# Kernel optimization log

Hardware: AMD Instinct MI355X
Metric: run time of the kernel (lower is better)

Reference implementation:

```python
import jax, jax.numpy as jnp
import numpy as np

C = 512
B, W, H = 16, 64, 64
K = 128


def setup_inputs() -> dict:
    key = jax.random.key(0)
    ks = jax.random.split(key, 17)
    s = 0.02
    inp = {
        "x1": jax.random.normal(ks[0], (B, C, W, H), jnp.float32),
        "y1": jax.random.normal(ks[1], (B, K, C), jnp.float32),
        "x2": jax.random.normal(ks[2], (B, C, W, H), jnp.float32),
        "y2": jax.random.normal(ks[3], (B, K, C), jnp.float32),
        # 1x1 conv weights stored as [out, in]
        "wq1": jax.random.normal(ks[4], (C // 4, C), jnp.float32) * s,
        "bq1": jnp.zeros((C // 4,), jnp.float32),
        "wq2": jax.random.normal(ks[5], (C // 4, C), jnp.float32) * s,
        "bq2": jnp.zeros((C // 4,), jnp.float32),
        "wk1": jax.random.normal(ks[6], (C // 2, C), jnp.float32) * s,
        "bk1": jnp.zeros((C // 2,), jnp.float32),
        "wk2": jax.random.normal(ks[7], (C // 2, C), jnp.float32) * s,
        "bk2": jnp.zeros((C // 2,), jnp.float32),
        "wv1": jax.random.normal(ks[8], (C, C), jnp.float32) * s,
        "bv1": jnp.zeros((C,), jnp.float32),
        "wv2": jax.random.normal(ks[9], (C, C), jnp.float32) * s,
        "bv2": jnp.zeros((C,), jnp.float32),
        "scale": jnp.ones((1,), jnp.float32) * 0.5,  # nn.Parameter(zeros) would kill grads; nonzero for testing
    }
    return inp


def reference(x1, y1, x2, y2, wq1, bq1, wq2, bq2, wk1, bk1, wk2, bk2,
              wv1, bv1, wv2, bv2, scale):
    b, c, w, h = x1.shape
    n = w * h
    # 1x1 convs == channel-wise linear maps
    q1 = jnp.einsum('bcwh,dc->bdwh', x1, wq1) + bq1[None, :, None, None]
    q2 = jnp.einsum('bcwh,dc->bdwh', x2, wq2) + bq2[None, :, None, None]
    # concat along channels -> [B, C/2, N] -> [B, N, C/2]
    q = jnp.concatenate([q1, q2], axis=1).reshape(b, c // 2, n).transpose(0, 2, 1)
    k1 = y1 @ wk1.T + bk1  # [B, K, C/2]
    k2 = y2 @ wk2.T + bk2
    v1 = y1 @ wv1.T + bv1  # [B, K, C]
    v2 = y2 @ wv2.T + bv2
    e1 = jnp.einsum('bnd,bkd->bnk', q, k1)  # [B, N, K]
    e2 = jnp.einsum('bnd,bkd->bnk', q, k2)
    attn = jax.nn.softmax(jnp.abs(e1 - e2), axis=-1)
    # out = value^T @ attn^T : [B, C, N]
    o1 = jnp.einsum('bkc,bnk->bcn', v1, attn).reshape(b, c, w, h)
    o2 = jnp.einsum('bkc,bnk->bcn', v2, attn).reshape(b, c, w, h)
    out1 = scale[0] * o1 + x1
    out2 = scale[0] * o2 + x2
    return out1, out2
```

## Files before the change

kernel.cpp:

```cpp
#include <hip/hip_runtime.h>

typedef unsigned short u16;
typedef __attribute__((ext_vector_type(8))) short short8v;
typedef __attribute__((ext_vector_type(4))) float floatx4;

#define B_ 16
#define C_ 512
#define N_ 4096
#define K_ 128
#define NT 64

__device__ __forceinline__ float bf2f(u16 u) {
    unsigned int x = ((unsigned int)u) << 16;
    return __builtin_bit_cast(float, x);
}
__device__ __forceinline__ u16 f2bf(float f) {
    unsigned int u = __builtin_bit_cast(unsigned int, f);
    u = u + 0x7FFFu + ((u >> 16) & 1u);
    return (u16)(u >> 16);
}

__global__ void conv_all(const float* __restrict__ y1, const float* __restrict__ y2,
                         const float* __restrict__ wk1, const float* __restrict__ wk2,
                         const float* __restrict__ wv1, const float* __restrict__ wv2,
                         const float* __restrict__ wq1, const float* __restrict__ wq2,
                         u16* y1b, u16* y2b, u16* wk1b, u16* wk2b, u16* wv1b, u16* wv2b,
                         u16* wq1t, u16* wq2t) {
    int tid = blockIdx.x * 256 + threadIdx.x;
    const int SY = B_ * K_ * C_;
    const int SWK = 256 * 512;
    const int SWV = 512 * 512;
    const int SQ = 128 * 512;
    int base = 2*SY + 2*SWK + 2*SWV;
    if (tid < base) {
        const float* src; u16* dst; int off;
        if (tid < SY)                 { src = y1;  dst = y1b;  off = tid; }
        else if (tid < 2*SY)          { src = y2;  dst = y2b;  off = tid - SY; }
        else if (tid < 2*SY+SWK)      { src = wk1; dst = wk1b; off = tid - 2*SY; }
        else if (tid < 2*SY+2*SWK)    { src = wk2; dst = wk2b; off = tid - 2*SY - SWK; }
        else if (tid < 2*SY+2*SWK+SWV){ src = wv1; dst = wv1b; off = tid - 2*SY - 2*SWK; }
        else                          { src = wv2; dst = wv2b; off = tid - 2*SY - 2*SWK - SWV; }
        dst[off] = f2bf(src[off]);
    } else {
        int e = tid - base;
        const float* s = (e >= SQ) ? wq2 : wq1;
        u16* d = (e >= SQ) ? wq2t : wq1t;
        e &= (SQ - 1);
        int dd = e >> 9;
        int c = e & 511;
        d[c * 128 + dd] = f2bf(s[dd * 512 + c]);
    }
}

__global__ void gemm_gkgv(const u16* __restrict__ y1b, const u16* __restrict__ y2b,
                          const u16* __restrict__ wk1b, const u16* __restrict__ wk2b,
                          const u16* __restrict__ wv1b, const u16* __restrict__ wv2b,
                          const float* __restrict__ bk1, const float* __restrict__ bk2,
                          const float* __restrict__ bv1, const float* __restrict__ bv2,
                          u16* k1b, u16* k2b, u16* vt1, u16* vt2) {
    int l = threadIdx.x;
    int id = blockIdx.x;
    const u16 *A, *Bt; const float* bias; u16* outp;
    int m0, n0, po; bool bias_m;
    if (id < 256) {
        int bx = id & 1, by = (id >> 1) & 3, z = id >> 3;
        int b = z >> 1, which = z & 1;
        A = (which ? y2b : y1b) + (size_t)b * K_ * C_;
        Bt = which ? wk2b : wk1b;
        bias = which ? bk2 : bk1;
        outp = (which ? k2b : k1b) + (size_t)b * K_ * 256;
        m0 = bx * 64; n0 = by * 64; po = 256; bias_m = false;
    } else {
        int id2 = id - 256;
        int bx = id2 & 7, by = (id2 >> 3) & 1, z = id2 >> 4;
        int b = z >> 1, which = z & 1;
        A = which ? wv2b : wv1b;
        Bt = (which ? y2b : y1b) + (size_t)b * K_ * C_;
        bias = which ? bv2 : bv1;
        outp = (which ? vt2 : vt1) + (size_t)b * C_ * K_;
        m0 = bx * 64; n0 = by * 64; po = 128; bias_m = true;
    }
    floatx4 acc[4][4] = {};
    for (int ch = 0; ch < 16; ++ch) {
        int koff = ch * 32 + (l >> 4) * 8;
        short8v a[4], wv[4];
#pragma unroll
        for (int mf = 0; mf < 4; ++mf) a[mf] = *(const short8v*)(A + (size_t)(m0 + mf*16 + (l & 15)) * 512 + koff);
#pragma unroll
        for (int nf = 0; nf < 4; ++nf) wv[nf] = *(const short8v*)(Bt + (size_t)(n0 + nf*16 + (l & 15)) * 512 + koff);
#pragma unroll
        for (int mf = 0; mf < 4; ++mf)
#pragma unroll
            for (int nf = 0; nf < 4; ++nf)
                acc[mf][nf] = __builtin_amdgcn_mfma_f32_16x16x32_bf16(a[mf], wv[nf], acc[mf][nf], 0, 0, 0);
    }
#pragma unroll
    for (int mf = 0; mf < 4; ++mf)
#pragma unroll
        for (int nf = 0; nf < 4; ++nf)
#pragma unroll
            for (int rg = 0; rg < 4; ++rg) {
                int m = m0 + mf*16 + (l >> 4)*4 + rg;
                int n = n0 + nf*16 + (l & 15);
                outp[(size_t)m * po + n] = f2bf(acc[mf][nf][rg] + (bias_m ? bias[m] : bias[n]));
            }
}

__global__ void kd_sub(const u16* __restrict__ k1b, const u16* __restrict__ k2b,
                       u16* kd) {
    int tid = blockIdx.x * 256 + threadIdx.x;
    kd[tid] = f2bf(bf2f(k1b[tid]) - bf2f(k2b[tid]));
}

__global__ void ebd_k(const u16* __restrict__ kd,
                      const float* __restrict__ bq1, const float* __restrict__ bq2,
                      float* ebd) {
    int tid = blockIdx.x * 256 + threadIdx.x;
    const u16* kb = kd + (size_t)tid * 256;
    float s = 0.f;
    for (int d = 0; d < 128; ++d) s += bq1[d] * bf2f(kb[d]);
    for (int d = 0; d < 128; ++d) s += bq2[d] * bf2f(kb[128 + d]);
    ebd[tid] = s;
}

__global__ void gemm_gkk(const u16* __restrict__ kd,
                         const u16* __restrict__ wq1t, const u16* __restrict__ wq2t,
                         u16* kkd1, u16* kkd2) {
    int l = threadIdx.x;
    int z = blockIdx.z; int b = z >> 1; int which = z & 1;
    const u16* A = kd + (size_t)b * K_ * 256 + which * 128;
    const u16* Wt = which ? wq2t : wq1t;
    u16* outp = (which ? kkd2 : kkd1) + (size_t)b * K_ * C_;
    int m0 = blockIdx.x * 64, n0 = blockIdx.y * 64;
    floatx4 acc[4][4] = {};
    for (int ch = 0; ch < 4; ++ch) {
        int koff = ch * 32 + (l >> 4) * 8;
        short8v a[4], wv[4];
#pragma unroll
        for (int mf = 0; mf < 4; ++mf) a[mf] = *(const short8v*)(A + (size_t)(m0 + mf*16 + (l & 15)) * 256 + koff);
#pragma unroll
        for (int nf = 0; nf < 4; ++nf) wv[nf] = *(const short8v*)(Wt + (size_t)(n0 + nf*16 + (l & 15)) * 128 + koff);
#pragma unroll
        for (int mf = 0; mf < 4; ++mf)
#pragma unroll
            for (int nf = 0; nf < 4; ++nf)
                acc[mf][nf] = __builtin_amdgcn_mfma_f32_16x16x32_bf16(a[mf], wv[nf], acc[mf][nf], 0, 0, 0);
    }
#pragma unroll
    for (int mf = 0; mf < 4; ++mf)
#pragma unroll
        for (int nf = 0; nf < 4; ++nf)
#pragma unroll
            for (int rg = 0; rg < 4; ++rg) {
                int m = m0 + mf*16 + (l >> 4)*4 + rg;
                int n = n0 + nf*16 + (l & 15);
                outp[(size_t)m * C_ + n] = f2bf(acc[mf][nf][rg]);
            }
}

__global__ __launch_bounds__(256, 3)
void main_attn(const float* __restrict__ x1, const float* __restrict__ x2,
               const u16* __restrict__ kkd1, const u16* __restrict__ kkd2,
               const u16* __restrict__ vt1, const u16* __restrict__ vt2,
               const float* __restrict__ ebd,
               const float* __restrict__ scale_p,
               float* __restrict__ out1, float* __restrict__ out2) {
    __shared__ u16 xTb[2][4096];
    __shared__ u16 attn_s[8192];
    __shared__ float redA[256];
    __shared__ float redM[64];

    int bid0 = blockIdx.x;
    int bid = ((bid0 & 7) << 7) | (bid0 >> 3);
    int b = bid >> 6;
    int n0 = (bid & 63) * NT;
    int t = threadIdx.x;
    int w = t >> 6;
    int l = t & 63;

    const float sc = scale_p[0];
    const float* xs0 = x1 + (size_t)b * C_ * N_;
    const float* xs1 = x2 + (size_t)b * C_ * N_;
    const u16* kkp[2] = { kkd1 + (size_t)b * K_ * C_, kkd2 + (size_t)b * K_ * C_ };

    floatx4 ed[4][2] = {};

    float pvA0[8], pvA1[8], pvB0[8], pvB1[8];
    short8v kkA[2][2], kkB[2][2];

    auto LOADX = [&](int r, float (&v0)[8], float (&v1)[8]) {
        const float* xp = (r >= 8 ? xs1 : xs0) + (size_t)((r & 7) * 64 + w * 16 + (l >> 5) * 8) * N_ + n0 + 2 * (l & 31);
#pragma unroll
        for (int j = 0; j < 8; ++j) { float2 f = *(const float2*)(xp + (size_t)j * N_); v0[j] = f.x; v1[j] = f.y; }
    };
    auto LOADK = [&](int r, short8v (&kkf)[2][2]) {
        const u16* base = kkp[r >> 3] + (size_t)(w * 32 + (l & 15)) * 512 + (r & 7) * 64 + (l >> 4) * 8;
#pragma unroll
        for (int kf = 0; kf < 2; ++kf)
#pragma unroll
            for (int ch = 0; ch < 2; ++ch)
                kkf[kf][ch] = *(const short8v*)(base + kf * 16 * 512 + ch * 32);
    };
    auto WRITEXT = [&](u16* xbuf, float (&v0)[8], float (&v1)[8]) {
        short8v p0, p1;
#pragma unroll
        for (int j = 0; j < 8; ++j) { p0[j] = (short)f2bf(v0[j]); p1[j] = (short)f2bf(v1[j]); }
        int row0 = 2 * (l & 31);
        int sw = 8 * ((w * 2 + (l >> 5)) ^ ((l & 31) & 7));
        *(short8v*)&xbuf[row0 * 64 + sw] = p0;
        *(short8v*)&xbuf[(row0 + 1) * 64 + sw] = p1;
    };
    auto EMM = [&](const u16* xbuf, short8v (&kkf)[2][2]) {
#pragma unroll
        for (int ch = 0; ch < 2; ++ch) {
            short8v a[4];
#pragma unroll
            for (int mf = 0; mf < 4; ++mf) {
                int row = mf * 16 + (l & 15);
                int g = ch * 4 + (l >> 4);
                a[mf] = *(const short8v*)&xbuf[row * 64 + 8 * (g ^ ((row >> 1) & 7))];
            }
#pragma unroll
            for (int kf = 0; kf < 2; ++kf)
#pragma unroll
                for (int mf = 0; mf < 4; ++mf)
                    ed[mf][kf] = __builtin_amdgcn_mfma_f32_16x16x32_bf16(a[mf], kkf[kf][ch], ed[mf][kf], 0, 0, 0);
        }
    };

    LOADX(0, pvA0, pvA1); LOADK(0, kkA);
    WRITEXT(xTb[0], pvA0, pvA1);
    LOADX(1, pvB0, pvB1); LOADK(1, kkB);
#pragma unroll
    for (int rr = 0; rr < 8; ++rr) {
        int rA = 2 * rr, rB = 2 * rr + 1;
        __syncthreads();
        EMM(xTb[0], kkA);
        WRITEXT(xTb[1], pvB0, pvB1);
        if (rA + 2 <= 15) { LOADX(rA + 2, pvA0, pvA1); LOADK(rA + 2, kkA); }
        __syncthreads();
        EMM(xTb[1], kkB);
        if (rB + 1 <= 15) WRITEXT(xTb[0], pvA0, pvA1);
        if (rB + 2 <= 15) { LOADX(rB + 2, pvB0, pvB1); LOADK(rB + 2, kkB); }
    }

    float ebdv[2];
#pragma unroll
    for (int kf = 0; kf < 2; ++kf) ebdv[kf] = ebd[b * 128 + w * 32 + kf * 16 + (l & 15)];
#pragma unroll
    for (int mf = 0; mf < 4; ++mf)
#pragma unroll
        for (int kf = 0; kf < 2; ++kf)
#pragma unroll
            for (int rg = 0; rg < 4; ++rg)
                ed[mf][kf][rg] = fabsf(ed[mf][kf][rg] + ebdv[kf]);

    float m16[16];
#pragma unroll
    for (int mf = 0; mf < 4; ++mf)
#pragma unroll
        for (int rg = 0; rg < 4; ++rg)
            m16[mf * 4 + rg] = fmaxf(ed[mf][0][rg], ed[mf][1][rg]);
#pragma unroll
    for (int st = 1; st < 16; st <<= 1)
#pragma unroll
        for (int i = 0; i < 16; ++i)
            m16[i] = fmaxf(m16[i], __shfl_xor(m16[i], st));
    if ((l & 15) == 0) {
#pragma unroll
        for (int mf = 0; mf < 4; ++mf)
#pragma unroll
            for (int rg = 0; rg < 4; ++rg)
                redA[w * 64 + mf * 16 + (l >> 4) * 4 + rg] = m16[mf * 4 + rg];
    }
    __syncthreads();
    if (t < 64) redM[t] = fmaxf(fmaxf(redA[t], redA[64 + t]), fmaxf(redA[128 + t], redA[192 + t]));
    __syncthreads();

    float s16[16];
#pragma unroll
    for (int mf = 0; mf < 4; ++mf)
#pragma unroll
        for (int rg = 0; rg < 4; ++rg) {
            float mr = redM[mf * 16 + (l >> 4) * 4 + rg];
            float e0 = __expf(ed[mf][0][rg] - mr);
            float e1 = __expf(ed[mf][1][rg] - mr);
            ed[mf][0][rg] = e0; ed[mf][1][rg] = e1;
            s16[mf * 4 + rg] = e0 + e1;
        }
#pragma unroll
    for (int st = 1; st < 16; st <<= 1)
#pragma unroll
        for (int i = 0; i < 16; ++i)
            s16[i] += __shfl_xor(s16[i], st);
    if ((l & 15) == 0) {
#pragma unroll
        for (int mf = 0; mf < 4; ++mf)
#pragma unroll
            for (int rg = 0; rg < 4; ++rg)
                redA[w * 64 + mf * 16 + (l >> 4) * 4 + rg] = s16[mf * 4 + rg];
    }
    __syncthreads();
    if (t < 64) redM[t] = redA[t] + redA[64 + t] + redA[128 + t] + redA[192 + t];
    __syncthreads();

#pragma unroll
    for (int mf = 0; mf < 4; ++mf)
#pragma unroll
        for (int rg = 0; rg < 4; ++rg) {
            int row = mf * 16 + (l >> 4) * 4 + rg;
            float inv = 1.0f / redM[row];
#pragma unroll
            for (int kf = 0; kf < 2; ++kf) {
                int col = w * 32 + kf * 16 + (l & 15);
                attn_s[row * 128 + 8 * ((col >> 3) ^ (row & 7)) + (col & 7)] = f2bf(ed[mf][kf][rg] * inv);
            }
        }
    __syncthreads();

    const u16* vt1p = vt1 + (size_t)b * C_ * K_;
    const u16* vt2p = vt2 + (size_t)b * C_ * K_;
    float* out1p = out1 + (size_t)b * C_ * N_;
    float* out2p = out2 + (size_t)b * C_ * N_;
    for (int q = 0; q < 8; ++q) {
        int oi = q >> 2, cc = q & 3;
        const u16* vt = oi ? vt2p : vt1p;
        const float* xr = oi ? xs1 : xs0;
        float* op = oi ? out2p : out1p;
        short8v vf[2][4];
#pragma unroll
        for (int mf = 0; mf < 2; ++mf)
#pragma unroll
            for (int kc = 0; kc < 4; ++kc)
                vf[mf][kc] = *(const short8v*)(vt + (size_t)(cc * 128 + w * 32 + mf * 16 + (l & 15)) * K_ + kc * 32 + (l >> 4) * 8);
        float resv[2][4][4];
#pragma unroll
        for (int mf = 0; mf < 2; ++mf)
#pragma unroll
            for (int rg = 0; rg < 4; ++rg)
#pragma unroll
                for (int nf = 0; nf < 4; ++nf)
                    resv[mf][rg][nf] = xr[(size_t)(cc * 128 + w * 32 + mf * 16 + (l >> 4) * 4 + rg) * N_ + n0 + nf * 16 + (l & 15)];
        floatx4 o[2][4] = {};
#pragma unroll
        for (int kc = 0; kc < 4; ++kc) {
            short8v bb[4];
#pragma unroll
            for (int nf = 0; nf < 4; ++nf) {
                int nrow = nf * 16 + (l & 15);
                int g = kc * 4 + (l >> 4);
                bb[nf] = *(const short8v*)&attn_s[nrow * 128 + 8 * (g ^ (nrow & 7))];
            }
#pragma unroll
            for (int nf = 0; nf < 4; ++nf)
#pragma unroll
                for (int mf = 0; mf < 2; ++mf)
                    o[mf][nf] = __builtin_amdgcn_mfma_f32_16x16x32_bf16(vf[mf][kc], bb[nf], o[mf][nf], 0, 0, 0);
        }
#pragma unroll
        for (int mf = 0; mf < 2; ++mf)
#pragma unroll
            for (int rg = 0; rg < 4; ++rg)
#pragma unroll
                for (int nf = 0; nf < 4; ++nf) {
                    size_t idx = (size_t)(cc * 128 + w * 32 + mf * 16 + (l >> 4) * 4 + rg) * N_ + n0 + nf * 16 + (l & 15);
                    op[idx] = sc * o[mf][nf][rg] + resv[mf][rg][nf];
                }
    }
}

extern "C" void kernel_launch(void* const* d_in, const int* in_sizes, int n_in,
                              void* d_out, int out_size, void* d_ws, size_t ws_size,
                              hipStream_t stream) {
    const float* x1 = (const float*)d_in[0];
    const float* y1 = (const float*)d_in[1];
    const float* x2 = (const float*)d_in[2];
    const float* y2 = (const float*)d_in[3];
    const float* wq1 = (const float*)d_in[4];
    const float* bq1 = (const float*)d_in[5];
    const float* wq2 = (const float*)d_in[6];
    const float* bq2 = (const float*)d_in[7];
    const float* wk1 = (const float*)d_in[8];
    const float* bk1 = (const float*)d_in[9];
    const float* wk2 = (const float*)d_in[10];
    const float* bk2 = (const float*)d_in[11];
    const float* wv1 = (const float*)d_in[12];
    const float* bv1 = (const float*)d_in[13];
    const float* wv2 = (const float*)d_in[14];
    const float* bv2 = (const float*)d_in[15];
    const float* scale = (const float*)d_in[16];

    char* ws = (char*)d_ws;
    u16* y1b  = (u16*)(ws + 0);
    u16* y2b  = (u16*)(ws + 2097152);
    u16* wk1b = (u16*)(ws + 4194304);
    u16* wk2b = (u16*)(ws + 4456448);
    u16* wv1b = (u16*)(ws + 4718592);
    u16* wv2b = (u16*)(ws + 5242880);
    u16* wq1t = (u16*)(ws + 5767168);
    u16* wq2t = (u16*)(ws + 5898240);
    u16* k1b  = (u16*)(ws + 6029312);
    u16* k2b  = (u16*)(ws + 7077888);
    u16* kd   = (u16*)(ws + 8126464);
    u16* kkd1 = (u16*)(ws + 9175040);
    u16* kkd2 = (u16*)(ws + 11272192);
    u16* vt1  = (u16*)(ws + 13369344);
    u16* vt2  = (u16*)(ws + 15466496);
    float* ebd = (float*)(ws + 17563648);

    float* out1 = (float*)d_out;
    float* out2 = out1 + (size_t)B_ * C_ * N_;

    hipLaunchKernelGGL(conv_all, dim3(11776), dim3(256), 0, stream,
                       y1, y2, wk1, wk2, wv1, wv2, wq1, wq2,
                       y1b, y2b, wk1b, wk2b, wv1b, wv2b, wq1t, wq2t);
    hipLaunchKernelGGL(gemm_gkgv, dim3(768), dim3(64), 0, stream,
                       y1b, y2b, wk1b, wk2b, wv1b, wv2b, bk1, bk2, bv1, bv2,
                       k1b, k2b, vt1, vt2);
    hipLaunchKernelGGL(kd_sub, dim3(2048), dim3(256), 0, stream, k1b, k2b, kd);
    hipLaunchKernelGGL(ebd_k, dim3(8), dim3(256), 0, stream, kd, bq1, bq2, ebd);
    hipLaunchKernelGGL(gemm_gkk, dim3(2, 8, 32), dim3(64), 0, stream,
                       kd, wq1t, wq2t, kkd1, kkd2);
    hipLaunchKernelGGL(main_attn, dim3(1024), dim3(256), 0, stream,
                       x1, x2, kkd1, kkd2, vt1, vt2, ebd, scale,
                       out1, out2);
}
```

Before: 240.5 us.

## Double main_attn block to 512 threads and software-pipeline the PV stage

Raises main_attn from 4 to 8 waves per block. Each wave now takes half the rows in the energy GEMM (split by nh/kg), and the PV output stage gives each wave one output tensor and channel group. The PV stage double-buffers V fragments and residual loads across 16-row steps so loads overlap MFMAs. The aim is more latency hiding and lower per-thread register pressure. The cost is more block-wide barriers among 8 waves and a different LDS swizzle and x-load pattern with per-lane scalar loads.

```diff
diff --git a/kernel.cpp b/kernel.cpp
--- a/kernel.cpp
+++ b/kernel.cpp
@@ -158,7 +158,7 @@
             }
 }
 
-__global__ __launch_bounds__(256, 3)
+__global__ __launch_bounds__(512, 4)
 void main_attn(const float* __restrict__ x1, const float* __restrict__ x2,
                const u16* __restrict__ kkd1, const u16* __restrict__ kkd2,
                const u16* __restrict__ vt1, const u16* __restrict__ vt2,
@@ -177,195 +177,200 @@
     int t = threadIdx.x;
     int w = t >> 6;
     int l = t & 63;
+    int nh = w >> 2;
+    int kg = w & 3;
 
     const float sc = scale_p[0];
     const float* xs0 = x1 + (size_t)b * C_ * N_;
     const float* xs1 = x2 + (size_t)b * C_ * N_;
     const u16* kkp[2] = { kkd1 + (size_t)b * K_ * C_, kkd2 + (size_t)b * K_ * C_ };
 
-    floatx4 ed[4][2] = {};
-
-    float pvA0[8], pvA1[8], pvB0[8], pvB1[8];
+    floatx4 ed[2][2] = {};
+
+    float xA[8], xB[8];
     short8v kkA[2][2], kkB[2][2];
 
-    auto LOADX = [&](int r, float (&v0)[8], float (&v1)[8]) {
-        const float* xp = (r >= 8 ? xs1 : xs0) + (size_t)((r & 7) * 64 + w * 16 + (l >> 5) * 8) * N_ + n0 + 2 * (l & 31);
-#pragma unroll
-        for (int j = 0; j < 8; ++j) { float2 f = *(const float2*)(xp + (size_t)j * N_); v0[j] = f.x; v1[j] = f.y; }
+    auto LOADX = [&](int r, float (&v)[8]) {
+        const float* xp = (r >= 8 ? xs1 : xs0) + (size_t)((r & 7) * 64 + w * 8) * N_ + n0 + l;
+#pragma unroll
+        for (int j = 0; j < 8; ++j) v[j] = xp[(size_t)j * N_];
+    };
+    auto WRITEXT = [&](u16* xbuf, float (&v)[8]) {
+        short8v p;
+#pragma unroll
+        for (int j = 0; j < 8; ++j) p[j] = (short)f2bf(v[j]);
+        *(short8v*)&xbuf[l * 64 + 8 * (w ^ (l & 7))] = p;
     };
     auto LOADK = [&](int r, short8v (&kkf)[2][2]) {
-        const u16* base = kkp[r >> 3] + (size_t)(w * 32 + (l & 15)) * 512 + (r & 7) * 64 + (l >> 4) * 8;
+        const u16* base = kkp[r >> 3] + (size_t)(kg * 32 + (l & 15)) * 512 + (r & 7) * 64 + (l >> 4) * 8;
 #pragma unroll
         for (int kf = 0; kf < 2; ++kf)
 #pragma unroll
             for (int ch = 0; ch < 2; ++ch)
                 kkf[kf][ch] = *(const short8v*)(base + kf * 16 * 512 + ch * 32);
     };
-    auto WRITEXT = [&](u16* xbuf, float (&v0)[8], float (&v1)[8]) {
-        short8v p0, p1;
-#pragma unroll
-        for (int j = 0; j < 8; ++j) { p0[j] = (short)f2bf(v0[j]); p1[j] = (short)f2bf(v1[j]); }
-        int row0 = 2 * (l & 31);
-        int sw = 8 * ((w * 2 + (l >> 5)) ^ ((l & 31) & 7));
-        *(short8v*)&xbuf[row0 * 64 + sw] = p0;
-        *(short8v*)&xbuf[(row0 + 1) * 64 + sw] = p1;
-    };
     auto EMM = [&](const u16* xbuf, short8v (&kkf)[2][2]) {
 #pragma unroll
         for (int ch = 0; ch < 2; ++ch) {
-            short8v a[4];
-#pragma unroll
-            for (int mf = 0; mf < 4; ++mf) {
-                int row = mf * 16 + (l & 15);
+            short8v a[2];
+#pragma unroll
+            for (int mf = 0; mf < 2; ++mf) {
+                int row = nh * 32 + mf * 16 + (l & 15);
                 int g = ch * 4 + (l >> 4);
-                a[mf] = *(const short8v*)&xbuf[row * 64 + 8 * (g ^ ((row >> 1) & 7))];
+                a[mf] = *(const short8v*)&xbuf[row * 64 + 8 * (g ^ (row & 7))];
             }
 #pragma unroll
             for (int kf = 0; kf < 2; ++kf)
 #pragma unroll
-                for (int mf = 0; mf < 4; ++mf)
+                for (int mf = 0; mf < 2; ++mf)
                     ed[mf][kf] = __builtin_amdgcn_mfma_f32_16x16x32_bf16(a[mf], kkf[kf][ch], ed[mf][kf], 0, 0, 0);
         }
     };
 
-    LOADX(0, pvA0, pvA1); LOADK(0, kkA);
-    WRITEXT(xTb[0], pvA0, pvA1);
-    LOADX(1, pvB0, pvB1); LOADK(1, kkB);
+    LOADX(0, xA); LOADK(0, kkA);
+    WRITEXT(xTb[0], xA);
+    LOADX(1, xB); LOADK(1, kkB);
 #pragma unroll
     for (int rr = 0; rr < 8; ++rr) {
         int rA = 2 * rr, rB = 2 * rr + 1;
         __syncthreads();
         EMM(xTb[0], kkA);
-        WRITEXT(xTb[1], pvB0, pvB1);
-        if (rA + 2 <= 15) { LOADX(rA + 2, pvA0, pvA1); LOADK(rA + 2, kkA); }
+        WRITEXT(xTb[1], xB);
+        if (rA + 2 <= 15) { LOADX(rA + 2, xA); LOADK(rA + 2, kkA); }
         __syncthreads();
         EMM(xTb[1], kkB);
-        if (rB + 1 <= 15) WRITEXT(xTb[0], pvA0, pvA1);
-        if (rB + 2 <= 15) { LOADX(rB + 2, pvB0, pvB1); LOADK(rB + 2, kkB); }
+        if (rB + 1 <= 15) WRITEXT(xTb[0], xA);
+        if (rB + 2 <= 15) { LOADX(rB + 2, xB); LOADK(rB + 2, kkB); }
     }
 
     float ebdv[2];
 #pragma unroll
-    for (int kf = 0; kf < 2; ++kf) ebdv[kf] = ebd[b * 128 + w * 32 + kf * 16 + (l & 15)];
-#pragma unroll
-    for (int mf = 0; mf < 4; ++mf)
+    for (int kf = 0; kf < 2; ++kf) ebdv[kf] = ebd[b * 128 + kg * 32 + kf * 16 + (l & 15)];
+#pragma unroll
+    for (int mf = 0; mf < 2; ++mf)
 #pragma unroll
         for (int kf = 0; kf < 2; ++kf)
 #pragma unroll
             for (int rg = 0; rg < 4; ++rg)
                 ed[mf][kf][rg] = fabsf(ed[mf][kf][rg] + ebdv[kf]);
 
-    float m16[16];
-#pragma unroll
-    for (int mf = 0; mf < 4; ++mf)
+    float m8[8];
+#pragma unroll
+    for (int mf = 0; mf < 2; ++mf)
 #pragma unroll
         for (int rg = 0; rg < 4; ++rg)
-            m16[mf * 4 + rg] = fmaxf(ed[mf][0][rg], ed[mf][1][rg]);
+            m8[mf * 4 + rg] = fmaxf(ed[mf][0][rg], ed[mf][1][rg]);
 #pragma unroll
     for (int st = 1; st < 16; st <<= 1)
 #pragma unroll
-        for (int i = 0; i < 16; ++i)
-            m16[i] = fmaxf(m16[i], __shfl_xor(m16[i], st));
+        for (int i = 0; i < 8; ++i)
+            m8[i] = fmaxf(m8[i], __shfl_xor(m8[i], st));
     if ((l & 15) == 0) {
 #pragma unroll
-        for (int mf = 0; mf < 4; ++mf)
+        for (int mf = 0; mf < 2; ++mf)
 #pragma unroll
             for (int rg = 0; rg < 4; ++rg)
-                redA[w * 64 + mf * 16 + (l >> 4) * 4 + rg] = m16[mf * 4 + rg];
+                redA[kg * 64 + nh * 32 + mf * 16 + (l >> 4) * 4 + rg] = m8[mf * 4 + rg];
     }
     __syncthreads();
     if (t < 64) redM[t] = fmaxf(fmaxf(redA[t], redA[64 + t]), fmaxf(redA[128 + t], redA[192 + t]));
     __syncthreads();
 
-    float s16[16];
-#pragma unroll
-    for (int mf = 0; mf < 4; ++mf)
+    float s8[8];
+#pragma unroll
+    for (int mf = 0; mf < 2; ++mf)
 #pragma unroll
         for (int rg = 0; rg < 4; ++rg) {
-            float mr = redM[mf * 16 + (l >> 4) * 4 + rg];
+            float mr = redM[nh * 32 + mf * 16 + (l >> 4) * 4 + rg];
             float e0 = __expf(ed[mf][0][rg] - mr);
             float e1 = __expf(ed[mf][1][rg] - mr);
             ed[mf][0][rg] = e0; ed[mf][1][rg] = e1;
-            s16[mf * 4 + rg] = e0 + e1;
+            s8[mf * 4 + rg] = e0 + e1;
         }
 #pragma unroll
     for (int st = 1; st < 16; st <<= 1)
 #pragma unroll
-        for (int i = 0; i < 16; ++i)
-            s16[i] += __shfl_xor(s16[i], st);
+        for (int i = 0; i < 8; ++i)
+            s8[i] += __shfl_xor(s8[i], st);
     if ((l & 15) == 0) {
 #pragma unroll
-        for (int mf = 0; mf < 4; ++mf)
+        for (int mf = 0; mf < 2; ++mf)
 #pragma unroll
             for (int rg = 0; rg < 4; ++rg)
-                redA[w * 64 + mf * 16 + (l >> 4) * 4 + rg] = s16[mf * 4 + rg];
+                redA[kg * 64 + nh * 32 + mf * 16 + (l >> 4) * 4 + rg] = s8[mf * 4 + rg];
     }
     __syncthreads();
     if (t < 64) redM[t] = redA[t] + redA[64 + t] + redA[128 + t] + redA[192 + t];
     __syncthreads();
 
 #pragma unroll
-    for (int mf = 0; mf < 4; ++mf)
+    for (int mf = 0; mf < 2; ++mf)
 #pragma unroll
         for (int rg = 0; rg < 4; ++rg) {
-            int row = mf * 16 + (l >> 4) * 4 + rg;
+            int row = nh * 32 + mf * 16 + (l >> 4) * 4 + rg;
             float inv = 1.0f / redM[row];
 #pragma unroll
             for (int kf = 0; kf < 2; ++kf) {
-                int col = w * 32 + kf * 16 + (l & 15);
+                int col = kg * 32 + kf * 16 + (l & 15);
                 attn_s[row * 128 + 8 * ((col >> 3) ^ (row & 7)) + (col & 7)] = f2bf(ed[mf][kf][rg] * inv);
             }
         }
     __syncthreads();
 
-    const u16* vt1p = vt1 + (size_t)b * C_ * K_;
-    const u16* vt2p = vt2 + (size_t)b * C_ * K_;
-    float* out1p = out1 + (size_t)b * C_ * N_;
-    float* out2p = out2 + (size_t)b * C_ * N_;
-    for (int q = 0; q < 8; ++q) {
-        int oi = q >> 2, cc = q & 3;
-        const u16* vt = oi ? vt2p : vt1p;
+    {
+        int oi = w >> 2, cg = w & 3;
+        const u16* vt = (oi ? vt2 : vt1) + (size_t)b * C_ * K_;
         const float* xr = oi ? xs1 : xs0;
-        float* op = oi ? out2p : out1p;
-        short8v vf[2][4];
-#pragma unroll
-        for (int mf = 0; mf < 2; ++mf)
-#pragma unroll
-            for (int kc = 0; kc < 4; ++kc)
-                vf[mf][kc] = *(const short8v*)(vt + (size_t)(cc * 128 + w * 32 + mf * 16 + (l & 15)) * K_ + kc * 32 + (l >> 4) * 8);
-        float resv[2][4][4];
-#pragma unroll
-        for (int mf = 0; mf < 2; ++mf)
+        float* op = (oi ? out2 : out1) + (size_t)b * C_ * N_;
+
+        short8v vfA[4], vfB[4];
+        float rsA[4][4], rsB[4][4];
+        auto LOADPV = [&](int step, short8v (&vf)[4], float (&rs)[4][4]) {
+            int cr = cg * 128 + step * 16;
+            const u16* vp = vt + (size_t)(cr + (l & 15)) * K_ + (l >> 4) * 8;
+#pragma unroll
+            for (int kc = 0; kc < 4; ++kc) vf[kc] = *(const short8v*)(vp + kc * 32);
+            const float* rp = xr + (size_t)(cr + (l >> 4) * 4) * N_ + n0 + (l & 15);
 #pragma unroll
             for (int rg = 0; rg < 4; ++rg)
 #pragma unroll
                 for (int nf = 0; nf < 4; ++nf)
-                    resv[mf][rg][nf] = xr[(size_t)(cc * 128 + w * 32 + mf * 16 + (l >> 4) * 4 + rg) * N_ + n0 + nf * 16 + (l & 15)];
-        floatx4 o[2][4] = {};
-#pragma unroll
-        for (int kc = 0; kc < 4; ++kc) {
-            short8v bb[4];
-#pragma unroll
-            for (int nf = 0; nf < 4; ++nf) {
-                int nrow = nf * 16 + (l & 15);
-                int g = kc * 4 + (l >> 4);
-                bb[nf] = *(const short8v*)&attn_s[nrow * 128 + 8 * (g ^ (nrow & 7))];
+                    rs[rg][nf] = rp[(size_t)rg * N_ + nf * 16];
+        };
+        auto COMPPV = [&](int step, short8v (&vf)[4], float (&rs)[4][4]) {
+            floatx4 o[4] = {};
+#pragma unroll
+            for (int kc = 0; kc < 4; ++kc) {
+                short8v bb[4];
+#pragma unroll
+                for (int nf = 0; nf < 4; ++nf) {
+                    int nrow = nf * 16 + (l & 15);
+                    int g = kc * 4 + (l >> 4);
+                    bb[nf] = *(const short8v*)&attn_s[nrow * 128 + 8 * (g ^ (nrow & 7))];
+                }
+#pragma unroll
+                for (int nf = 0; nf < 4; ++nf)
+                    o[nf] = __builtin_amdgcn_mfma_f32_16x16x32_bf16(vf[kc], bb[nf], o[nf], 0, 0, 0);
             }
-#pragma unroll
-            for (int nf = 0; nf < 4; ++nf)
-#pragma unroll
-                for (int mf = 0; mf < 2; ++mf)
-                    o[mf][nf] = __builtin_amdgcn_mfma_f32_16x16x32_bf16(vf[mf][kc], bb[nf], o[mf][nf], 0, 0, 0);
+            int cr = cg * 128 + step * 16 + (l >> 4) * 4;
+#pragma unroll
+            for (int rg = 0; rg < 4; ++rg)
+#pragma unroll
+                for (int nf = 0; nf < 4; ++nf) {
+                    size_t idx = (size_t)(cr + rg) * N_ + n0 + nf * 16 + (l & 15);
+                    op[idx] = sc * o[nf][rg] + rs[rg][nf];
+                }
+        };
+
+        LOADPV(0, vfA, rsA);
+        LOADPV(1, vfB, rsB);
+#pragma unroll
+        for (int ss = 0; ss < 4; ++ss) {
+            COMPPV(2 * ss, vfA, rsA);
+            if (2 * ss + 2 < 8) LOADPV(2 * ss + 2, vfA, rsA);
+            COMPPV(2 * ss + 1, vfB, rsB);
+            if (2 * ss + 3 < 8) LOADPV(2 * ss + 3, vfB, rsB);
         }
-#pragma unroll
-        for (int mf = 0; mf < 2; ++mf)
-#pragma unroll
-            for (int rg = 0; rg < 4; ++rg)
-#pragma unroll
-                for (int nf = 0; nf < 4; ++nf) {
-                    size_t idx = (size_t)(cc * 128 + w * 32 + mf * 16 + (l >> 4) * 4 + rg) * N_ + n0 + nf * 16 + (l & 15);
-                    op[idx] = sc * o[mf][nf][rg] + resv[mf][rg][nf];
-                }
     }
 }
 
@@ -421,7 +426,7 @@
     hipLaunchKernelGGL(ebd_k, dim3(8), dim3(256), 0, stream, kd, bq1, bq2, ebd);
     hipLaunchKernelGGL(gemm_gkk, dim3(2, 8, 32), dim3(64), 0, stream,
                        kd, wq1t, wq2t, kkd1, kkd2);
-    hipLaunchKernelGGL(main_attn, dim3(1024), dim3(256), 0, stream,
+    hipLaunchKernelGGL(main_attn, dim3(1024), dim3(512), 0, stream,
                        x1, x2, kkd1, kkd2, vt1, vt2, ebd, scale,
                        out1, out2);
 }
```

Result: slower. 459.7 us (+91.1%).
